# Kernel optimization log

Hardware: AMD Instinct MI355X
Metric: run time of the kernel (lower is better)

The kernel has to match this reference:

```python
import jax, jax.numpy as jnp
import numpy as np

# Segment geometry (from init_kwargs): modes ['u','uv','v'] -> out_v = alpha * x_u @ W_uv
U = 128
V = 128
IN_OFF = [0, 128, 256, 384]
W_OFF = [k * U * V for k in range(8)]          # [0,16384,...,114688]
OUT_OFF = [0, 128, 256, 384]
IN_STRIDE = 512
OUT_STRIDE = 512
W_STRIDE = 8 * U * V                           # 131072
# (in_seg, w_seg, out_seg, coefficient)
PATHS = [(0, 0, 0, 1.0), (1, 1, 1, 1.0), (2, 2, 2, 1.0), (3, 3, 3, 1.0),
         (0, 4, 1, 0.5), (1, 5, 2, 0.5), (2, 6, 3, 0.5), (3, 7, 0, 0.5)]
B = 32768
E = 4  # num_embeddings (experts)


def setup_inputs() -> dict:
    key = jax.random.key(0)
    k1, k2, k3 = jax.random.split(key, 3)
    tensor_in = jax.random.normal(k1, (B, IN_STRIDE), dtype=jnp.float32)
    tensor_w = jax.random.normal(k2, (E, W_STRIDE), dtype=jnp.float32)
    tensor_w_id = jax.random.randint(k3, (B,), 0, E, dtype=jnp.int32)
    return {"tensor_in": tensor_in, "tensor_w": tensor_w, "tensor_w_id": tensor_w_id}


def _batch_linear(tensor_in, tensor_w, tensor_w_id):
    """Segmented path-indexed grouped linear (cuEquivariance BatchLinear fwd).

    tensor_in: [B, IN_STRIDE]; tensor_w: [E, W_STRIDE]; tensor_w_id: [B] int in [0,E).
    For each path (i, j, k, alpha):
        out[b, OUT_OFF[k]:+V] += alpha * x[b, IN_OFF[i]:+U] @ W[w_id[b], seg j].reshape(U, V)
    """
    nb = tensor_in.shape[0]
    ne = tensor_w.shape[0]
    onehot = jax.nn.one_hot(tensor_w_id, ne, dtype=tensor_in.dtype)  # [B, E]
    out = jnp.zeros((nb, OUT_STRIDE), dtype=tensor_in.dtype)
    for (i, j, k, a) in PATHS:
        x = tensor_in[:, IN_OFF[i]:IN_OFF[i] + U]                    # [B, U]
        w_seg = tensor_w[:, W_OFF[j]:W_OFF[j] + U * V].reshape(ne, U, V)
        # masked per-expert dense GEMMs (small fixed expert count)
        y = jnp.zeros((nb, V), dtype=tensor_in.dtype)
        for e in range(ne):
            y = y + onehot[:, e:e + 1] * (x @ w_seg[e])              # [B, V]
        out = out.at[:, OUT_OFF[k]:OUT_OFF[k] + V].add(a * y)
    return out


def reference(tensor_in, tensor_w, tensor_w_id):
    return _batch_linear(tensor_in, tensor_w, tensor_w_id)
```

## Files before the change

### kernel.cpp

```cpp
#include <hip/hip_runtime.h>
#include <stdint.h>

#define U 128
#define V 128
#define IN_STRIDE 512
#define OUT_STRIDE 512
#define W_STRIDE (8 * U * V)
#define NB 32768

#define WS_WSHUF 0
#define WS_PERM  (1 << 20)
#define WS_CURS  ((1 << 20) + (1 << 19))

typedef __bf16 bf16x8 __attribute__((ext_vector_type(8)));
typedef float f32x16 __attribute__((ext_vector_type(16)));
typedef unsigned int u32x4 __attribute__((ext_vector_type(4)));
typedef unsigned int u32x2 __attribute__((ext_vector_type(2)));

static __device__ __forceinline__ unsigned short f2bf(float f) {
    unsigned int u = __builtin_bit_cast(unsigned int, f);
    u += 0x7FFFu + ((u >> 16) & 1u);
    return (unsigned short)(u >> 16);
}

__global__ void prep_kernel(const float* __restrict__ w, const int* __restrict__ wid,
                            unsigned short* __restrict__ wshuf, int* __restrict__ cursors,
                            int* __restrict__ perm) {
    int blk = blockIdx.x;
    if (blk < 256) {
        int t = blk * 256 + threadIdx.x;
        int lane = t & 63;
        int kt = (t >> 6) & 7;
        int nt = (t >> 9) & 3;
        int s  = (t >> 11) & 7;
        int e  = (t >> 14) & 3;
        int kbase = kt * 16 + ((lane >> 5) << 3);
        int n = nt * 32 + (lane & 31);
        const float* src = w + (size_t)e * W_STRIDE + (size_t)s * (U * V) + n;
        float sc = (s >= 4) ? 0.5f : 1.0f;
        __attribute__((aligned(16))) unsigned short o[8];
#pragma unroll
        for (int j = 0; j < 8; j++) o[j] = f2bf(src[(size_t)(kbase + j) * V] * sc);
        *(u32x4*)(wshuf + (size_t)t * 8) = *(const u32x4*)o;
    } else {
        __shared__ int lcnt[4], lbase[4];
        int tid = threadIdx.x;
        if (tid < 4) lcnt[tid] = 0;
        __syncthreads();
        int b = (blk - 256) * 256 + tid;
        int e = wid[b];
        int r = atomicAdd(&lcnt[e], 1);
        __syncthreads();
        if (tid < 4) lbase[tid] = atomicAdd(&cursors[tid], lcnt[tid]);
        __syncthreads();
        perm[e * NB + lbase[e] + r] = b;
    }
}

__global__ __launch_bounds__(512) void gemm_kernel(
        const float* __restrict__ x, const unsigned short* __restrict__ wshuf,
        const int* __restrict__ cursors, const int* __restrict__ perm,
        float* __restrict__ out) {
    int c4_0 = cursors[0], c4_1 = cursors[1], c4_2 = cursors[2], c4_3 = cursors[3];
    int cnts[4] = {c4_0, c4_1, c4_2, c4_3};
    int g = blockIdx.x;
    int e = -1, tile = 0, acc = 0;
#pragma unroll
    for (int i = 0; i < 4; i++) {
        int te = (cnts[i] + 31) >> 5;
        if (e < 0 && g < acc + te) { e = i; tile = g - acc; }
        acc += te;
    }
    if (e < 0) return;
    int cnt = cnts[e];
    int rows = cnt - tile * 32;
    if (rows > 32) rows = 32;
    int tbase = e * NB + tile * 32;

    __shared__ unsigned short lds[32 * 512];
    __shared__ int s_perm[32];

    int t = threadIdx.x;

    {
        int r = t >> 4;
        int gg = t & 15;
        bool valid = (r < rows);
        int row_g = valid ? perm[tbase + r] : 0;
        if (gg == 0) s_perm[r] = row_g;
        const float* xr = x + (size_t)row_g * IN_STRIDE;
#pragma unroll
        for (int i = 0; i < 8; i++) {
            int c = gg * 4 + i * 64;
            float4 v = valid ? *(const float4*)(xr + c) : make_float4(0.f, 0.f, 0.f, 0.f);
            __attribute__((aligned(8))) unsigned short h[4];
            h[0] = f2bf(v.x); h[1] = f2bf(v.y); h[2] = f2bf(v.z); h[3] = f2bf(v.w);
            int off = r * 512 + ((((c >> 3) ^ (r & 7))) << 3) + (c & 7);
            *(u32x2*)(lds + off) = *(const u32x2*)h;
        }
    }
    __syncthreads();

    int w = t >> 6;
    int lane = t & 63;
    int kout = w >> 1;
    int nhalf = w & 1;

    f32x16 acc0 = {}, acc1 = {};

    int xb[2]; int sg[2];
    xb[0] = kout;            sg[0] = kout;
    xb[1] = (kout + 3) & 3;  sg[1] = xb[1] + 4;

    const int m0 = lane & 31;
    const int khalf = (lane >> 5) << 3;
    const int rowswz = (m0 & 7);

#pragma unroll
    for (int c = 0; c < 2; c++) {
        int colbase = xb[c] * 128;
        const unsigned short* wseg =
            wshuf + (((size_t)(e * 8 + sg[c]) * 4 + nhalf * 2) * 8) * 64 * 8;
#pragma unroll
        for (int kt = 0; kt < 8; kt++) {
            int kabs = colbase + kt * 16 + khalf;
            int packoff = (((kabs >> 3) ^ rowswz) << 3);
            bf16x8 a0 = __builtin_bit_cast(bf16x8, *(const u32x4*)(lds + m0 * 512 + packoff));
            bf16x8 b0 = __builtin_bit_cast(bf16x8, *(const u32x4*)(wseg + ((size_t)(kt) * 64 + lane) * 8));
            bf16x8 b1 = __builtin_bit_cast(bf16x8, *(const u32x4*)(wseg + ((size_t)(8 + kt) * 64 + lane) * 8));
            acc0 = __builtin_amdgcn_mfma_f32_32x32x16_bf16(a0, b0, acc0, 0, 0, 0);
            acc1 = __builtin_amdgcn_mfma_f32_32x32x16_bf16(a0, b1, acc1, 0, 0, 0);
        }
    }

    int colb = kout * 128 + nhalf * 64 + (lane & 31);
    int rh = (lane >> 5) << 2;
#pragma unroll
    for (int q = 0; q < 4; q++) {
#pragma unroll
        for (int d = 0; d < 4; d++) {
            int reg = q * 4 + d;
            int rl = d + 8 * q + rh;
            if (rl < rows) {
                int rg = s_perm[rl];
                out[(size_t)rg * OUT_STRIDE + colb]      = acc0[reg];
                out[(size_t)rg * OUT_STRIDE + colb + 32] = acc1[reg];
            }
        }
    }
}

extern "C" void kernel_launch(void* const* d_in, const int* in_sizes, int n_in,
                              void* d_out, int out_size, void* d_ws, size_t ws_size,
                              hipStream_t stream) {
    const float* x = (const float*)d_in[0];
    const float* w = (const float*)d_in[1];
    const int* wid = (const int*)d_in[2];
    float* out = (float*)d_out;

    char* ws = (char*)d_ws;
    unsigned short* wshuf = (unsigned short*)(ws + WS_WSHUF);
    int* perm = (int*)(ws + WS_PERM);
    int* cursors = (int*)(ws + WS_CURS);

    hipMemsetAsync(cursors, 0, 16, stream);
    prep_kernel<<<384, 256, 0, stream>>>(w, wid, wshuf, cursors, perm);
    gemm_kernel<<<1027, 512, 0, stream>>>(x, wshuf, cursors, perm, out);
}
```

Before: 136.2 us.

## Make GEMM kernel persistent with double-buffered LDS and register prefetch of next tile

The GEMM kernel becomes a grid-stride persistent loop over 512 blocks instead of one block per 32-row tile. While the current tile runs its MFMAs, the next tile's gathered x rows are prefetched into registers, and two LDS buffers alternate between tiles. The aim is to hide global gather latency behind compute and cut per-block launch overhead. In exchange, register pressure and LDS use double (64KB LDS per block), which may lower occupancy. There is also only one barrier per iteration, so the buffer reuse two iterations later relies on that barrier for ordering.

```diff
diff --git a/kernel.cpp b/kernel.cpp
--- a/kernel.cpp
+++ b/kernel.cpp
@@ -61,92 +61,133 @@
         const float* __restrict__ x, const unsigned short* __restrict__ wshuf,
         const int* __restrict__ cursors, const int* __restrict__ perm,
         float* __restrict__ out) {
-    int c4_0 = cursors[0], c4_1 = cursors[1], c4_2 = cursors[2], c4_3 = cursors[3];
-    int cnts[4] = {c4_0, c4_1, c4_2, c4_3};
+    const int c0 = cursors[0], c1 = cursors[1], c2 = cursors[2], c3 = cursors[3];
+    const int te0 = (c0 + 31) >> 5, te1 = (c1 + 31) >> 5,
+              te2 = (c2 + 31) >> 5, te3 = (c3 + 31) >> 5;
+    const int ntot = te0 + te1 + te2 + te3;
+
+    __shared__ unsigned short lds[2][32 * 512];
+    __shared__ int s_perm[2][32];
+
+    const int t = threadIdx.x;
+    const int r = t >> 4;
+    const int gg = t & 15;
+
+    const int w = t >> 6, lane = t & 63;
+    const int kout = w >> 1, nhalf = w & 1;
+    const int m0 = lane & 31;
+    const int khalf = (lane >> 5) << 3;
+    const int rowswz = m0 & 7;
+    const int xb0 = kout, sg0 = kout;
+    const int xb1 = (kout + 3) & 3, sg1 = xb1 + 4;
+    const int colb = kout * 128 + nhalf * 64 + m0;
+    const int rh = (lane >> 5) << 2;
+
+    auto map = [&](int g, int& e, int& rows, int& tbase) {
+        int cs[4] = {c0, c1, c2, c3};
+        int tes[4] = {te0, te1, te2, te3};
+        int acc = 0; e = -1; rows = 0; tbase = 0;
+#pragma unroll
+        for (int i = 0; i < 4; i++) {
+            if (e < 0 && g < acc + tes[i]) {
+                e = i;
+                int tile = g - acc;
+                rows = cs[i] - tile * 32;
+                if (rows > 32) rows = 32;
+                tbase = i * NB + tile * 32;
+            }
+            acc += tes[i];
+        }
+    };
+
     int g = blockIdx.x;
-    int e = -1, tile = 0, acc = 0;
-#pragma unroll
-    for (int i = 0; i < 4; i++) {
-        int te = (cnts[i] + 31) >> 5;
-        if (e < 0 && g < acc + te) { e = i; tile = g - acc; }
-        acc += te;
-    }
-    if (e < 0) return;
-    int cnt = cnts[e];
-    int rows = cnt - tile * 32;
-    if (rows > 32) rows = 32;
-    int tbase = e * NB + tile * 32;
-
-    __shared__ unsigned short lds[32 * 512];
-    __shared__ int s_perm[32];
-
-    int t = threadIdx.x;
-
+    if (g >= ntot) return;
+    int e_c, rows_c, tb_c;
+    map(g, e_c, rows_c, tb_c);
+
+    float4 pf[8];
+    bool val = (r < rows_c);
+    int rowg = val ? perm[tb_c + r] : 0;
     {
-        int r = t >> 4;
-        int gg = t & 15;
-        bool valid = (r < rows);
-        int row_g = valid ? perm[tbase + r] : 0;
-        if (gg == 0) s_perm[r] = row_g;
-        const float* xr = x + (size_t)row_g * IN_STRIDE;
+        const float* xr = x + (size_t)rowg * IN_STRIDE;
 #pragma unroll
         for (int i = 0; i < 8; i++) {
             int c = gg * 4 + i * 64;
-            float4 v = valid ? *(const float4*)(xr + c) : make_float4(0.f, 0.f, 0.f, 0.f);
-            __attribute__((aligned(8))) unsigned short h[4];
-            h[0] = f2bf(v.x); h[1] = f2bf(v.y); h[2] = f2bf(v.z); h[3] = f2bf(v.w);
-            int off = r * 512 + ((((c >> 3) ^ (r & 7))) << 3) + (c & 7);
-            *(u32x2*)(lds + off) = *(const u32x2*)h;
+            if (val) pf[i] = *(const float4*)(xr + c);
         }
     }
-    __syncthreads();
-
-    int w = t >> 6;
-    int lane = t & 63;
-    int kout = w >> 1;
-    int nhalf = w & 1;
-
-    f32x16 acc0 = {}, acc1 = {};
-
-    int xb[2]; int sg[2];
-    xb[0] = kout;            sg[0] = kout;
-    xb[1] = (kout + 3) & 3;  sg[1] = xb[1] + 4;
-
-    const int m0 = lane & 31;
-    const int khalf = (lane >> 5) << 3;
-    const int rowswz = (m0 & 7);
-
-#pragma unroll
-    for (int c = 0; c < 2; c++) {
-        int colbase = xb[c] * 128;
-        const unsigned short* wseg =
-            wshuf + (((size_t)(e * 8 + sg[c]) * 4 + nhalf * 2) * 8) * 64 * 8;
-#pragma unroll
-        for (int kt = 0; kt < 8; kt++) {
-            int kabs = colbase + kt * 16 + khalf;
-            int packoff = (((kabs >> 3) ^ rowswz) << 3);
-            bf16x8 a0 = __builtin_bit_cast(bf16x8, *(const u32x4*)(lds + m0 * 512 + packoff));
-            bf16x8 b0 = __builtin_bit_cast(bf16x8, *(const u32x4*)(wseg + ((size_t)(kt) * 64 + lane) * 8));
-            bf16x8 b1 = __builtin_bit_cast(bf16x8, *(const u32x4*)(wseg + ((size_t)(8 + kt) * 64 + lane) * 8));
-            acc0 = __builtin_amdgcn_mfma_f32_32x32x16_bf16(a0, b0, acc0, 0, 0, 0);
-            acc1 = __builtin_amdgcn_mfma_f32_32x32x16_bf16(a0, b1, acc1, 0, 0, 0);
-        }
-    }
-
-    int colb = kout * 128 + nhalf * 64 + (lane & 31);
-    int rh = (lane >> 5) << 2;
-#pragma unroll
-    for (int q = 0; q < 4; q++) {
-#pragma unroll
-        for (int d = 0; d < 4; d++) {
-            int reg = q * 4 + d;
-            int rl = d + 8 * q + rh;
-            if (rl < rows) {
-                int rg = s_perm[rl];
-                out[(size_t)rg * OUT_STRIDE + colb]      = acc0[reg];
-                out[(size_t)rg * OUT_STRIDE + colb + 32] = acc1[reg];
-            }
-        }
+
+    int buf = 0;
+    while (true) {
+        {
+            unsigned short* L = lds[buf];
+#pragma unroll
+            for (int i = 0; i < 8; i++) {
+                int c = gg * 4 + i * 64;
+                float4 v = val ? pf[i] : make_float4(0.f, 0.f, 0.f, 0.f);
+                __attribute__((aligned(8))) unsigned short h[4];
+                h[0] = f2bf(v.x); h[1] = f2bf(v.y); h[2] = f2bf(v.z); h[3] = f2bf(v.w);
+                int off = r * 512 + ((((c >> 3) ^ (r & 7))) << 3) + (c & 7);
+                *(u32x2*)(L + off) = *(const u32x2*)h;
+            }
+            if (gg == 0) s_perm[buf][r] = rowg;
+        }
+        __syncthreads();
+
+        int gn = g + gridDim.x;
+        int e_n = -1, rows_n = 0, tb_n = 0;
+        if (gn < ntot) {
+            map(gn, e_n, rows_n, tb_n);
+            bool vn = (r < rows_n);
+            int rn = vn ? perm[tb_n + r] : 0;
+            const float* xr = x + (size_t)rn * IN_STRIDE;
+#pragma unroll
+            for (int i = 0; i < 8; i++) {
+                int c = gg * 4 + i * 64;
+                if (vn) pf[i] = *(const float4*)(xr + c);
+            }
+            rowg = rn; val = vn;
+        }
+
+        const unsigned short* L = lds[buf];
+        f32x16 acc0 = {}, acc1 = {};
+        {
+            int xbs[2] = {xb0, xb1};
+            int sgs[2] = {sg0, sg1};
+#pragma unroll
+            for (int c = 0; c < 2; c++) {
+                int colbase = xbs[c] * 128;
+                const unsigned short* wseg =
+                    wshuf + (((size_t)(e_c * 8 + sgs[c]) * 4 + nhalf * 2) * 8) * 64 * 8;
+#pragma unroll
+                for (int kt = 0; kt < 8; kt++) {
+                    int kabs = colbase + kt * 16 + khalf;
+                    int packoff = (((kabs >> 3) ^ rowswz) << 3);
+                    bf16x8 a0 = __builtin_bit_cast(bf16x8, *(const u32x4*)(L + m0 * 512 + packoff));
+                    bf16x8 b0 = __builtin_bit_cast(bf16x8, *(const u32x4*)(wseg + ((size_t)(kt) * 64 + lane) * 8));
+                    bf16x8 b1 = __builtin_bit_cast(bf16x8, *(const u32x4*)(wseg + ((size_t)(8 + kt) * 64 + lane) * 8));
+                    acc0 = __builtin_amdgcn_mfma_f32_32x32x16_bf16(a0, b0, acc0, 0, 0, 0);
+                    acc1 = __builtin_amdgcn_mfma_f32_32x32x16_bf16(a0, b1, acc1, 0, 0, 0);
+                }
+            }
+        }
+
+#pragma unroll
+        for (int q = 0; q < 4; q++) {
+#pragma unroll
+            for (int d = 0; d < 4; d++) {
+                int reg = q * 4 + d;
+                int rl = d + 8 * q + rh;
+                if (rl < rows_c) {
+                    int rg = s_perm[buf][rl];
+                    out[(size_t)rg * OUT_STRIDE + colb]      = acc0[reg];
+                    out[(size_t)rg * OUT_STRIDE + colb + 32] = acc1[reg];
+                }
+            }
+        }
+
+        if (e_n < 0) break;
+        e_c = e_n; rows_c = rows_n; tb_c = tb_n; g = gn; buf ^= 1;
     }
 }
 
@@ -165,5 +206,5 @@
 
     hipMemsetAsync(cursors, 0, 16, stream);
     prep_kernel<<<384, 256, 0, stream>>>(w, wid, wshuf, cursors, perm);
-    gemm_kernel<<<1027, 512, 0, stream>>>(x, wshuf, cursors, perm, out);
-}
+    gemm_kernel<<<512, 512, 0, stream>>>(x, wshuf, cursors, perm, out);
+}
```

New measurement: 134.8 us. About the same (-1.0%).

## Replace expert sort/gather with masked dense GEMM over all experts

Applied to the files above, without the earlier changes.

Drops the per-expert permutation (memset, atomics, perm writes and gathered row loads and stores). Each block now takes 64 contiguous rows and runs the MFMA for all four experts, zeroing A rows that belong to other experts, which is algebraically the same as the reference's one-hot masked sum. This removes one launch, the sorting step and scattered memory access. In exchange it does four times the matrix FLOPs and four times the weight reads per tile, and uses larger 64-row tiles with a launch-bounds occupancy hint.

```diff
diff --git a/kernel.cpp b/kernel.cpp
--- a/kernel.cpp
+++ b/kernel.cpp
@@ -9,8 +9,6 @@
 #define NB 32768
 
 #define WS_WSHUF 0
-#define WS_PERM  (1 << 20)
-#define WS_CURS  ((1 << 20) + (1 << 19))
 
 typedef __bf16 bf16x8 __attribute__((ext_vector_type(8)));
 typedef float f32x16 __attribute__((ext_vector_type(16)));
@@ -23,129 +21,117 @@
     return (unsigned short)(u >> 16);
 }
 
-__global__ void prep_kernel(const float* __restrict__ w, const int* __restrict__ wid,
-                            unsigned short* __restrict__ wshuf, int* __restrict__ cursors,
-                            int* __restrict__ perm) {
-    int blk = blockIdx.x;
-    if (blk < 256) {
-        int t = blk * 256 + threadIdx.x;
-        int lane = t & 63;
-        int kt = (t >> 6) & 7;
-        int nt = (t >> 9) & 3;
-        int s  = (t >> 11) & 7;
-        int e  = (t >> 14) & 3;
-        int kbase = kt * 16 + ((lane >> 5) << 3);
-        int n = nt * 32 + (lane & 31);
-        const float* src = w + (size_t)e * W_STRIDE + (size_t)s * (U * V) + n;
-        float sc = (s >= 4) ? 0.5f : 1.0f;
-        __attribute__((aligned(16))) unsigned short o[8];
+__global__ void prep_kernel(const float* __restrict__ w, unsigned short* __restrict__ wshuf) {
+    int t = blockIdx.x * 256 + threadIdx.x;
+    int lane = t & 63;
+    int kt = (t >> 6) & 7;
+    int nt = (t >> 9) & 3;
+    int s  = (t >> 11) & 7;
+    int e  = (t >> 14) & 3;
+    int kbase = kt * 16 + ((lane >> 5) << 3);
+    int n = nt * 32 + (lane & 31);
+    const float* src = w + (size_t)e * W_STRIDE + (size_t)s * (U * V) + n;
+    float sc = (s >= 4) ? 0.5f : 1.0f;
+    __attribute__((aligned(16))) unsigned short o[8];
 #pragma unroll
-        for (int j = 0; j < 8; j++) o[j] = f2bf(src[(size_t)(kbase + j) * V] * sc);
-        *(u32x4*)(wshuf + (size_t)t * 8) = *(const u32x4*)o;
-    } else {
-        __shared__ int lcnt[4], lbase[4];
-        int tid = threadIdx.x;
-        if (tid < 4) lcnt[tid] = 0;
-        __syncthreads();
-        int b = (blk - 256) * 256 + tid;
-        int e = wid[b];
-        int r = atomicAdd(&lcnt[e], 1);
-        __syncthreads();
-        if (tid < 4) lbase[tid] = atomicAdd(&cursors[tid], lcnt[tid]);
-        __syncthreads();
-        perm[e * NB + lbase[e] + r] = b;
-    }
+    for (int j = 0; j < 8; j++) o[j] = f2bf(src[(size_t)(kbase + j) * V] * sc);
+    *(u32x4*)(wshuf + (size_t)t * 8) = *(const u32x4*)o;
 }
 
-__global__ __launch_bounds__(512) void gemm_kernel(
+__global__ __launch_bounds__(512, 4) void gemm_kernel(
         const float* __restrict__ x, const unsigned short* __restrict__ wshuf,
-        const int* __restrict__ cursors, const int* __restrict__ perm,
-        float* __restrict__ out) {
-    int c4_0 = cursors[0], c4_1 = cursors[1], c4_2 = cursors[2], c4_3 = cursors[3];
-    int cnts[4] = {c4_0, c4_1, c4_2, c4_3};
-    int g = blockIdx.x;
-    int e = -1, tile = 0, acc = 0;
-#pragma unroll
-    for (int i = 0; i < 4; i++) {
-        int te = (cnts[i] + 31) >> 5;
-        if (e < 0 && g < acc + te) { e = i; tile = g - acc; }
-        acc += te;
-    }
-    if (e < 0) return;
-    int cnt = cnts[e];
-    int rows = cnt - tile * 32;
-    if (rows > 32) rows = 32;
-    int tbase = e * NB + tile * 32;
+        const int* __restrict__ wid, float* __restrict__ out) {
+    const int rowbase = blockIdx.x * 64;
+    __shared__ unsigned short lds[64 * 512];
 
-    __shared__ unsigned short lds[32 * 512];
-    __shared__ int s_perm[32];
-
-    int t = threadIdx.x;
+    const int t = threadIdx.x;
 
     {
-        int r = t >> 4;
-        int gg = t & 15;
-        bool valid = (r < rows);
-        int row_g = valid ? perm[tbase + r] : 0;
-        if (gg == 0) s_perm[r] = row_g;
-        const float* xr = x + (size_t)row_g * IN_STRIDE;
+        int r = t >> 3;
+        int g = t & 7;
+        const float* xr = x + (size_t)(rowbase + r) * IN_STRIDE;
+        unsigned short* Lrow = lds + r * 512;
+        int rs = r & 7;
 #pragma unroll
-        for (int i = 0; i < 8; i++) {
-            int c = gg * 4 + i * 64;
-            float4 v = valid ? *(const float4*)(xr + c) : make_float4(0.f, 0.f, 0.f, 0.f);
+        for (int i = 0; i < 16; i++) {
+            int c = g * 4 + i * 32;
+            float4 v = *(const float4*)(xr + c);
             __attribute__((aligned(8))) unsigned short h[4];
             h[0] = f2bf(v.x); h[1] = f2bf(v.y); h[2] = f2bf(v.z); h[3] = f2bf(v.w);
-            int off = r * 512 + ((((c >> 3) ^ (r & 7))) << 3) + (c & 7);
-            *(u32x2*)(lds + off) = *(const u32x2*)h;
+            int off = ((((c >> 3) ^ rs)) << 3) + (c & 7);
+            *(u32x2*)(Lrow + off) = *(const u32x2*)h;
         }
     }
+
+    const int w = t >> 6, lane = t & 63;
+    const int kout = w >> 1, nhalf = w & 1;
+    const int m0 = lane & 31;
+    const int khalf3 = (lane >> 5);
+    const int rowswz = m0 & 7;
+
+    const int e0 = wid[rowbase + m0];
+    const int e1 = wid[rowbase + m0 + 32];
+
     __syncthreads();
 
-    int w = t >> 6;
-    int lane = t & 63;
-    int kout = w >> 1;
-    int nhalf = w & 1;
+    unsigned int msk0[4], msk1[4];
+#pragma unroll
+    for (int e = 0; e < 4; e++) {
+        msk0[e] = (e0 == e) ? 0xFFFFFFFFu : 0u;
+        msk1[e] = (e1 == e) ? 0xFFFFFFFFu : 0u;
+    }
 
-    f32x16 acc0 = {}, acc1 = {};
+    f32x16 acc00 = {}, acc01 = {}, acc10 = {}, acc11 = {};
 
-    int xb[2]; int sg[2];
-    xb[0] = kout;            sg[0] = kout;
-    xb[1] = (kout + 3) & 3;  sg[1] = xb[1] + 4;
+    const int xbs0 = kout, xbs1 = (kout + 3) & 3;
+    const int sgs0 = kout, sgs1 = xbs1 + 4;
+    int xbs[2] = {xbs0, xbs1};
+    int sgs[2] = {sgs0, sgs1};
 
-    const int m0 = lane & 31;
-    const int khalf = (lane >> 5) << 3;
-    const int rowswz = (m0 & 7);
+    const unsigned short* Lr0 = lds + m0 * 512;
+    const unsigned short* Lr1 = lds + (m0 + 32) * 512;
 
 #pragma unroll
     for (int c = 0; c < 2; c++) {
-        int colbase = xb[c] * 128;
-        const unsigned short* wseg =
-            wshuf + (((size_t)(e * 8 + sg[c]) * 4 + nhalf * 2) * 8) * 64 * 8;
+        int colbase3 = xbs[c] * 16;
 #pragma unroll
         for (int kt = 0; kt < 8; kt++) {
-            int kabs = colbase + kt * 16 + khalf;
-            int packoff = (((kabs >> 3) ^ rowswz) << 3);
-            bf16x8 a0 = __builtin_bit_cast(bf16x8, *(const u32x4*)(lds + m0 * 512 + packoff));
-            bf16x8 b0 = __builtin_bit_cast(bf16x8, *(const u32x4*)(wseg + ((size_t)(kt) * 64 + lane) * 8));
-            bf16x8 b1 = __builtin_bit_cast(bf16x8, *(const u32x4*)(wseg + ((size_t)(8 + kt) * 64 + lane) * 8));
-            acc0 = __builtin_amdgcn_mfma_f32_32x32x16_bf16(a0, b0, acc0, 0, 0, 0);
-            acc1 = __builtin_amdgcn_mfma_f32_32x32x16_bf16(a0, b1, acc1, 0, 0, 0);
+            int kabs3 = colbase3 + kt * 2 + khalf3;
+            int packoff = ((kabs3 ^ rowswz) << 3);
+            u32x4 a0u = *(const u32x4*)(Lr0 + packoff);
+            u32x4 a1u = *(const u32x4*)(Lr1 + packoff);
+#pragma unroll
+            for (int e = 0; e < 4; e++) {
+                const unsigned short* wseg =
+                    wshuf + ((size_t)((e * 8 + sgs[c]) * 4 + nhalf * 2) * 8) * 512;
+                bf16x8 b0 = __builtin_bit_cast(bf16x8, *(const u32x4*)(wseg + (size_t)kt * 512 + lane * 8));
+                bf16x8 b1 = __builtin_bit_cast(bf16x8, *(const u32x4*)(wseg + (size_t)(8 + kt) * 512 + lane * 8));
+                u32x4 mm0 = {msk0[e], msk0[e], msk0[e], msk0[e]};
+                u32x4 mm1 = {msk1[e], msk1[e], msk1[e], msk1[e]};
+                bf16x8 a0m = __builtin_bit_cast(bf16x8, a0u & mm0);
+                bf16x8 a1m = __builtin_bit_cast(bf16x8, a1u & mm1);
+                acc00 = __builtin_amdgcn_mfma_f32_32x32x16_bf16(a0m, b0, acc00, 0, 0, 0);
+                acc01 = __builtin_amdgcn_mfma_f32_32x32x16_bf16(a0m, b1, acc01, 0, 0, 0);
+                acc10 = __builtin_amdgcn_mfma_f32_32x32x16_bf16(a1m, b0, acc10, 0, 0, 0);
+                acc11 = __builtin_amdgcn_mfma_f32_32x32x16_bf16(a1m, b1, acc11, 0, 0, 0);
+            }
         }
     }
 
-    int colb = kout * 128 + nhalf * 64 + (lane & 31);
-    int rh = (lane >> 5) << 2;
+    const int colb = kout * 128 + nhalf * 64 + m0;
+    const int rh = (lane >> 5) << 2;
 #pragma unroll
     for (int q = 0; q < 4; q++) {
 #pragma unroll
         for (int d = 0; d < 4; d++) {
             int reg = q * 4 + d;
             int rl = d + 8 * q + rh;
-            if (rl < rows) {
-                int rg = s_perm[rl];
-                out[(size_t)rg * OUT_STRIDE + colb]      = acc0[reg];
-                out[(size_t)rg * OUT_STRIDE + colb + 32] = acc1[reg];
-            }
+            float* o0 = out + (size_t)(rowbase + rl) * OUT_STRIDE + colb;
+            float* o1 = out + (size_t)(rowbase + rl + 32) * OUT_STRIDE + colb;
+            o0[0]  = acc00[reg];
+            o0[32] = acc01[reg];
+            o1[0]  = acc10[reg];
+            o1[32] = acc11[reg];
         }
     }
 }
@@ -158,12 +144,8 @@
     const int* wid = (const int*)d_in[2];
     float* out = (float*)d_out;
 
-    char* ws = (char*)d_ws;
-    unsigned short* wshuf = (unsigned short*)(ws + WS_WSHUF);
-    int* perm = (int*)(ws + WS_PERM);
-    int* cursors = (int*)(ws + WS_CURS);
+    unsigned short* wshuf = (unsigned short*)((char*)d_ws + WS_WSHUF);
 
-    hipMemsetAsync(cursors, 0, 16, stream);
-    prep_kernel<<<384, 256, 0, stream>>>(w, wid, wshuf, cursors, perm);
-    gemm_kernel<<<1027, 512, 0, stream>>>(x, wshuf, cursors, perm, out);
+    prep_kernel<<<256, 256, 0, stream>>>(w, wshuf);
+    gemm_kernel<<<512, 512, 0, stream>>>(x, wshuf, wid, out);
 }
```

Measured after the change: 134.6 us. Within noise of the previous version (-1.1%).

## Pre-shuffle gathered activations to bf16 MFMA layout in separate kernel; drop LDS staging

Applied to the files above, without the earlier changes.

Adds a kernel that gathers the permuted input rows, converts them to bf16 and writes them in an MFMA-fragment-ready layout in workspace. The GEMM kernel then loads A fragments directly from global memory with no LDS or barrier, and uses 4 waves each computing a full 128-column output slab with four accumulators instead of 8 waves with two. The cost is an extra kernel launch and an extra round trip of bf16 activations through global memory. In exchange the GEMM kernel gets lower LDS usage and potentially higher occupancy.

```diff
diff --git a/kernel.cpp b/kernel.cpp
--- a/kernel.cpp
+++ b/kernel.cpp
@@ -7,20 +7,39 @@
 #define OUT_STRIDE 512
 #define W_STRIDE (8 * U * V)
 #define NB 32768
+#define MAXTILES 1027
 
 #define WS_WSHUF 0
 #define WS_PERM  (1 << 20)
 #define WS_CURS  ((1 << 20) + (1 << 19))
+#define WS_XSHUF (2 << 20)
 
 typedef __bf16 bf16x8 __attribute__((ext_vector_type(8)));
 typedef float f32x16 __attribute__((ext_vector_type(16)));
 typedef unsigned int u32x4 __attribute__((ext_vector_type(4)));
-typedef unsigned int u32x2 __attribute__((ext_vector_type(2)));
 
 static __device__ __forceinline__ unsigned short f2bf(float f) {
     unsigned int u = __builtin_bit_cast(unsigned int, f);
     u += 0x7FFFu + ((u >> 16) & 1u);
     return (unsigned short)(u >> 16);
+}
+
+static __device__ __forceinline__ void tile_map(int g, int c0, int c1, int c2, int c3,
+                                                int& e, int& rows, int& tbase) {
+    int cs[4] = {c0, c1, c2, c3};
+    int acc = 0; e = -1; rows = 0; tbase = 0;
+#pragma unroll
+    for (int i = 0; i < 4; i++) {
+        int te = (cs[i] + 31) >> 5;
+        if (e < 0 && g < acc + te) {
+            e = i;
+            int tile = g - acc;
+            rows = cs[i] - tile * 32;
+            if (rows > 32) rows = 32;
+            tbase = i * NB + tile * 32;
+        }
+        acc += te;
+    }
 }
 
 __global__ void prep_kernel(const float* __restrict__ w, const int* __restrict__ wid,
@@ -57,94 +76,92 @@
     }
 }
 
-__global__ __launch_bounds__(512) void gemm_kernel(
-        const float* __restrict__ x, const unsigned short* __restrict__ wshuf,
+__global__ __launch_bounds__(256, 4) void xshuf_kernel(
+        const float* __restrict__ x, const int* __restrict__ perm,
+        const int* __restrict__ cursors, unsigned short* __restrict__ xshuf) {
+    int t = blockIdx.x * 256 + threadIdx.x;
+    int tile = t >> 11;
+    int rem = t & 2047;
+    int ktile = rem >> 6;
+    int lane = rem & 63;
+    int c0 = cursors[0], c1 = cursors[1], c2 = cursors[2], c3 = cursors[3];
+    int e, rows, tbase;
+    tile_map(tile, c0, c1, c2, c3, e, rows, tbase);
+    int m = lane & 31;
+    __attribute__((aligned(16))) unsigned short o[8] = {0, 0, 0, 0, 0, 0, 0, 0};
+    if (e >= 0 && m < rows) {
+        int row = perm[tbase + m];
+        const float* p = x + (size_t)row * IN_STRIDE + ktile * 16 + ((lane >> 5) << 3);
+        float4 v0 = *(const float4*)p;
+        float4 v1 = *(const float4*)(p + 4);
+        o[0] = f2bf(v0.x); o[1] = f2bf(v0.y); o[2] = f2bf(v0.z); o[3] = f2bf(v0.w);
+        o[4] = f2bf(v1.x); o[5] = f2bf(v1.y); o[6] = f2bf(v1.z); o[7] = f2bf(v1.w);
+    }
+    *(u32x4*)(xshuf + (size_t)t * 8) = *(const u32x4*)o;
+}
+
+__global__ __launch_bounds__(256, 4) void gemm_kernel(
+        const unsigned short* __restrict__ xshuf, const unsigned short* __restrict__ wshuf,
         const int* __restrict__ cursors, const int* __restrict__ perm,
         float* __restrict__ out) {
-    int c4_0 = cursors[0], c4_1 = cursors[1], c4_2 = cursors[2], c4_3 = cursors[3];
-    int cnts[4] = {c4_0, c4_1, c4_2, c4_3};
+    int c0 = cursors[0], c1 = cursors[1], c2 = cursors[2], c3 = cursors[3];
     int g = blockIdx.x;
-    int e = -1, tile = 0, acc = 0;
-#pragma unroll
-    for (int i = 0; i < 4; i++) {
-        int te = (cnts[i] + 31) >> 5;
-        if (e < 0 && g < acc + te) { e = i; tile = g - acc; }
-        acc += te;
-    }
+    int e, rows, tbase;
+    tile_map(g, c0, c1, c2, c3, e, rows, tbase);
     if (e < 0) return;
-    int cnt = cnts[e];
-    int rows = cnt - tile * 32;
-    if (rows > 32) rows = 32;
-    int tbase = e * NB + tile * 32;
 
-    __shared__ unsigned short lds[32 * 512];
-    __shared__ int s_perm[32];
+    const int t = threadIdx.x;
+    const int kout = t >> 6;
+    const int lane = t & 63;
+    const int m0 = lane & 31;
 
-    int t = threadIdx.x;
+    const unsigned short* xs = xshuf + (size_t)g * 16384;
 
-    {
-        int r = t >> 4;
-        int gg = t & 15;
-        bool valid = (r < rows);
-        int row_g = valid ? perm[tbase + r] : 0;
-        if (gg == 0) s_perm[r] = row_g;
-        const float* xr = x + (size_t)row_g * IN_STRIDE;
-#pragma unroll
-        for (int i = 0; i < 8; i++) {
-            int c = gg * 4 + i * 64;
-            float4 v = valid ? *(const float4*)(xr + c) : make_float4(0.f, 0.f, 0.f, 0.f);
-            __attribute__((aligned(8))) unsigned short h[4];
-            h[0] = f2bf(v.x); h[1] = f2bf(v.y); h[2] = f2bf(v.z); h[3] = f2bf(v.w);
-            int off = r * 512 + ((((c >> 3) ^ (r & 7))) << 3) + (c & 7);
-            *(u32x2*)(lds + off) = *(const u32x2*)h;
-        }
-    }
-    __syncthreads();
+    f32x16 acc0 = {}, acc1 = {}, acc2 = {}, acc3 = {};
 
-    int w = t >> 6;
-    int lane = t & 63;
-    int kout = w >> 1;
-    int nhalf = w & 1;
-
-    f32x16 acc0 = {}, acc1 = {};
-
-    int xb[2]; int sg[2];
-    xb[0] = kout;            sg[0] = kout;
-    xb[1] = (kout + 3) & 3;  sg[1] = xb[1] + 4;
-
-    const int m0 = lane & 31;
-    const int khalf = (lane >> 5) << 3;
-    const int rowswz = (m0 & 7);
+    const int xb0 = kout, sg0 = kout;
+    const int xb1 = (kout + 3) & 3, sg1 = xb1 + 4;
+    int xbs[2] = {xb0, xb1};
+    int sgs[2] = {sg0, sg1};
 
 #pragma unroll
     for (int c = 0; c < 2; c++) {
-        int colbase = xb[c] * 128;
-        const unsigned short* wseg =
-            wshuf + (((size_t)(e * 8 + sg[c]) * 4 + nhalf * 2) * 8) * 64 * 8;
+        const unsigned short* wbase = wshuf + (size_t)(e * 8 + sgs[c]) * 16384;
+        const int Kbase = xbs[c] * 8;
 #pragma unroll
         for (int kt = 0; kt < 8; kt++) {
-            int kabs = colbase + kt * 16 + khalf;
-            int packoff = (((kabs >> 3) ^ rowswz) << 3);
-            bf16x8 a0 = __builtin_bit_cast(bf16x8, *(const u32x4*)(lds + m0 * 512 + packoff));
-            bf16x8 b0 = __builtin_bit_cast(bf16x8, *(const u32x4*)(wseg + ((size_t)(kt) * 64 + lane) * 8));
-            bf16x8 b1 = __builtin_bit_cast(bf16x8, *(const u32x4*)(wseg + ((size_t)(8 + kt) * 64 + lane) * 8));
-            acc0 = __builtin_amdgcn_mfma_f32_32x32x16_bf16(a0, b0, acc0, 0, 0, 0);
-            acc1 = __builtin_amdgcn_mfma_f32_32x32x16_bf16(a0, b1, acc1, 0, 0, 0);
+            bf16x8 a = __builtin_bit_cast(bf16x8,
+                *(const u32x4*)(xs + ((size_t)(Kbase + kt) * 64 + lane) * 8));
+            bf16x8 b0 = __builtin_bit_cast(bf16x8,
+                *(const u32x4*)(wbase + ((size_t)(0 * 8 + kt) * 64 + lane) * 8));
+            bf16x8 b1 = __builtin_bit_cast(bf16x8,
+                *(const u32x4*)(wbase + ((size_t)(1 * 8 + kt) * 64 + lane) * 8));
+            bf16x8 b2 = __builtin_bit_cast(bf16x8,
+                *(const u32x4*)(wbase + ((size_t)(2 * 8 + kt) * 64 + lane) * 8));
+            bf16x8 b3 = __builtin_bit_cast(bf16x8,
+                *(const u32x4*)(wbase + ((size_t)(3 * 8 + kt) * 64 + lane) * 8));
+            acc0 = __builtin_amdgcn_mfma_f32_32x32x16_bf16(a, b0, acc0, 0, 0, 0);
+            acc1 = __builtin_amdgcn_mfma_f32_32x32x16_bf16(a, b1, acc1, 0, 0, 0);
+            acc2 = __builtin_amdgcn_mfma_f32_32x32x16_bf16(a, b2, acc2, 0, 0, 0);
+            acc3 = __builtin_amdgcn_mfma_f32_32x32x16_bf16(a, b3, acc3, 0, 0, 0);
         }
     }
 
-    int colb = kout * 128 + nhalf * 64 + (lane & 31);
-    int rh = (lane >> 5) << 2;
+    const int rh = (lane >> 5) << 2;
+    const int colb = kout * 128 + m0;
 #pragma unroll
     for (int q = 0; q < 4; q++) {
 #pragma unroll
         for (int d = 0; d < 4; d++) {
-            int reg = q * 4 + d;
             int rl = d + 8 * q + rh;
             if (rl < rows) {
-                int rg = s_perm[rl];
-                out[(size_t)rg * OUT_STRIDE + colb]      = acc0[reg];
-                out[(size_t)rg * OUT_STRIDE + colb + 32] = acc1[reg];
+                int rg = perm[tbase + rl];
+                float* o = out + (size_t)rg * OUT_STRIDE + colb;
+                int reg = q * 4 + d;
+                o[0]  = acc0[reg];
+                o[32] = acc1[reg];
+                o[64] = acc2[reg];
+                o[96] = acc3[reg];
             }
         }
     }
@@ -162,8 +179,10 @@
     unsigned short* wshuf = (unsigned short*)(ws + WS_WSHUF);
     int* perm = (int*)(ws + WS_PERM);
     int* cursors = (int*)(ws + WS_CURS);
+    unsigned short* xshuf = (unsigned short*)(ws + WS_XSHUF);
 
     hipMemsetAsync(cursors, 0, 16, stream);
     prep_kernel<<<384, 256, 0, stream>>>(w, wid, wshuf, cursors, perm);
-    gemm_kernel<<<1027, 512, 0, stream>>>(x, wshuf, cursors, perm, out);
+    xshuf_kernel<<<MAXTILES * 8, 256, 0, stream>>>(x, perm, cursors, xshuf);
+    gemm_kernel<<<MAXTILES, 256, 0, stream>>>(xshuf, wshuf, cursors, perm, out);
 }
```

Result: slower. 154.9 us (+13.8%).
